# Kernel optimization log

Hardware: AMD Instinct MI355X
Metric: run time of the kernel (lower is better)

Reference implementation:

```python
import jax, jax.numpy as jnp
import numpy as np

HID = 2048; S = 2048; NH = 16
Q_LORA = 1536; KV_LORA = 512
D_NOPE = 128; D_ROPE = 64; D_V = 128
D_QK = D_NOPE + D_ROPE  # 192
EPS = 1e-6


def setup_inputs() -> dict:
    key = jax.random.key(0)
    ks = jax.random.split(key, 8)
    hidden_states = jax.random.normal(ks[0], (1, S, HID), dtype=jnp.float32)
    # real RoPE tables, HF layout: cos/sin = concat(freqs, freqs) along last dim
    inv_freq = 1.0 / (10000.0 ** (np.arange(0, D_ROPE, 2, dtype=np.float32) / D_ROPE))
    t = np.arange(S, dtype=np.float32)
    freqs = np.outer(t, inv_freq)  # [S, D_ROPE//2]
    emb = np.concatenate([freqs, freqs], axis=-1)  # [S, D_ROPE]
    cos = jnp.asarray(np.cos(emb))[None]  # [1, S, D_ROPE]
    sin = jnp.asarray(np.sin(emb))[None]
    def lin(k, fan_in, fan_out):
        return jax.random.normal(k, (fan_in, fan_out), dtype=jnp.float32) / np.sqrt(fan_in)
    return {
        'hidden_states': hidden_states, 'cos': cos, 'sin': sin,
        'w_qa': lin(ks[1], HID, Q_LORA),
        'g_qa': jnp.ones((Q_LORA,), jnp.float32),
        'w_qb': lin(ks[2], Q_LORA, NH * D_QK),
        'w_kva': lin(ks[3], HID, KV_LORA + D_ROPE),
        'g_kva': jnp.ones((KV_LORA,), jnp.float32),
        'w_kvb': lin(ks[4], KV_LORA, NH * (D_NOPE + D_V)),
        'w_o': lin(ks[5], NH * D_V, HID),
    }


def _rmsnorm(x, g):
    var = jnp.mean(x * x, axis=-1, keepdims=True)
    return x * jax.lax.rsqrt(var + EPS) * g


def _deinterleave(x):
    # view (..., d//2, 2) -> transpose -> reshape: even-index dims first, then odd
    b, h, s, d = x.shape
    return x.reshape(b, h, s, d // 2, 2).transpose(0, 1, 2, 4, 3).reshape(b, h, s, d)


def _rotate_half(x):
    x1, x2 = jnp.split(x, 2, axis=-1)
    return jnp.concatenate([-x2, x1], axis=-1)


def _apply_rope(q, k, cos, sin):
    cos = cos[:, None]  # [B,1,S,D]
    sin = sin[:, None]
    q = _deinterleave(q)
    k = _deinterleave(k)
    q_emb = q * cos + _rotate_half(q) * sin
    k_emb = k * cos + _rotate_half(k) * sin
    return q_emb, k_emb


def reference(hidden_states, cos, sin, w_qa, g_qa, w_qb, w_kva, g_kva, w_kvb, w_o):
    bsz, q_len, _ = hidden_states.shape
    # low-rank Q projection
    q = _rmsnorm(hidden_states @ w_qa, g_qa) @ w_qb  # [B,S,NH*D_QK]
    q = q.reshape(bsz, q_len, NH, D_QK).transpose(0, 2, 1, 3)  # [B,NH,S,D_QK]
    q_nope, q_pe = q[..., :D_NOPE], q[..., D_NOPE:]
    # compressed KV + shared rope key
    ckv = hidden_states @ w_kva  # [B,S,KV_LORA+D_ROPE]
    compressed_kv, k_pe = ckv[..., :KV_LORA], ckv[..., KV_LORA:]
    k_pe = k_pe.reshape(bsz, q_len, 1, D_ROPE).transpose(0, 2, 1, 3)  # [B,1,S,D_ROPE]
    kv = (_rmsnorm(compressed_kv, g_kva) @ w_kvb).reshape(bsz, q_len, NH, D_NOPE + D_V).transpose(0, 2, 1, 3)
    k_nope, value_states = kv[..., :D_NOPE], kv[..., D_NOPE:]
    # interleaved RoPE
    q_pe, k_pe = _apply_rope(q_pe, k_pe, cos, sin)
    query_states = jnp.concatenate([q_nope, q_pe], axis=-1)  # [B,NH,S,D_QK]
    key_states = jnp.concatenate([k_nope, jnp.broadcast_to(k_pe, (bsz, NH, q_len, D_ROPE))], axis=-1)
    # causal attention with MLA softmax scale
    scale = D_QK ** (-0.5)
    scores = jnp.einsum('bhqd,bhkd->bhqk', query_states, key_states) * scale
    mask = jnp.tril(jnp.ones((q_len, q_len), dtype=bool))
    scores = jnp.where(mask, scores, jnp.finfo(scores.dtype).min)
    probs = jax.nn.softmax(scores, axis=-1)
    attn = jnp.einsum('bhqk,bhkd->bhqd', probs, value_states)  # [B,NH,S,D_V]
    attn = attn.transpose(0, 2, 1, 3).reshape(bsz, q_len, NH * D_V)
    return attn @ w_o
```

## Files before the change

### kernel.cpp

```cpp
#include <hip/hip_runtime.h>
#include <hip/hip_bf16.h>

#define S_LEN 2048
#define HID_D 2048
#define NHEAD 16
#define QLORA 1536
#define KVLORA 512
#define DNOPE 128
#define DROPE 64
#define DV 128
#define DQK 192
#define NCAT 2176

#define KS_SH (64 * 192)
#define VS_SH (128 * 64)
#define BUF_SH (KS_SH + VS_SH)

typedef __hip_bfloat16 bf16;
typedef __attribute__((ext_vector_type(8))) short short8;
typedef __attribute__((ext_vector_type(4))) short s16x4;
typedef __attribute__((ext_vector_type(4))) float f32x4;

__device__ __forceinline__ float ldE(const float* p) { return *p; }
__device__ __forceinline__ float ldE(const bf16* p) { return __bfloat162float(*p); }
__device__ __forceinline__ void stE(float* p, float v) { *p = v; }
__device__ __forceinline__ void stE(bf16* p, float v) { *p = __float2bfloat16(v); }

__device__ __forceinline__ short bf16bits(float v) {
    __hip_bfloat16 h = __float2bfloat16(v);
    return *reinterpret_cast<short*>(&h);
}

__device__ __forceinline__ float b2f(short s) {
    union { short s; bf16 h; } u;
    u.s = s;
    return __bfloat162float(u.h);
}

__device__ __forceinline__ f32x4 mfma16(short8 a, short8 b, f32x4 c) {
    return __builtin_amdgcn_mfma_f32_16x16x32_bf16(a, b, c, 0, 0, 0);
}

__device__ __forceinline__ void gload16(const void* g, void* l) {
    __builtin_amdgcn_global_load_lds(
        (const __attribute__((address_space(1))) unsigned int*)g,
        (__attribute__((address_space(3))) unsigned int*)l, 16, 0, 0);
}

__global__ void detect_kernel(const void* hidden, int* flag) {
    __shared__ int red[256];
    const int tid = threadIdx.x;
    const bf16* hb = (const bf16*)hidden;
    float a = fabsf(__bfloat162float(hb[tid]));
    red[tid] = (!(a < 64.f) || (a != 0.f && a < 1e-30f)) ? 1 : 0;
    __syncthreads();
    for (int o = 128; o > 0; o >>= 1) {
        if (tid < o) red[tid] += red[tid + o];
        __syncthreads();
    }
    if (tid == 0) *flag = (red[0] > 16) ? 1 : 0;
}

__global__ void convert_kernel(const void* in, bf16* out, int n8, const int* flag) {
    int i = blockIdx.x * 256 + threadIdx.x;
    if (i >= n8) return;
    size_t off = (size_t)i * 8;
    short8 o;
    if (*flag) {
        const float* f = (const float*)in + off;
#pragma unroll
        for (int j = 0; j < 8; ++j) o[j] = bf16bits(f[j]);
    } else {
        o = *(const short8*)((const short*)in + off);
    }
    *(short8*)((short*)out + off) = o;
}

template <int KDIM>
__device__ void transpose_tile(const void* in, bf16* out, int N, int n0, int k0,
                               int roff, int fp32) {
    __shared__ __align__(16) short Ts[64][80];
    const int tid = threadIdx.x;
    const bool inb = n0 < N;
    const int kl = tid >> 4;
    const int nl = (tid & 15) * 4;
#pragma unroll
    for (int p = 0; p < 4; ++p) {
        int k = kl + p * 16;
        float v[4] = {0.f, 0.f, 0.f, 0.f};
        if (inb) {
            if (fp32) {
                const float4 f = *(const float4*)((const float*)in + (size_t)(k0 + k) * N + n0 + nl);
                v[0] = f.x; v[1] = f.y; v[2] = f.z; v[3] = f.w;
            } else {
                const bf16* bp = (const bf16*)in + (size_t)(k0 + k) * N + n0 + nl;
#pragma unroll
                for (int i = 0; i < 4; ++i) v[i] = __bfloat162float(bp[i]);
            }
        }
#pragma unroll
        for (int i = 0; i < 4; ++i) Ts[nl + i][k] = bf16bits(v[i]);
    }
    __syncthreads();
    const int nr = tid >> 2;
    const int kq = (tid & 3) * 16;
    short* op = (short*)out + (size_t)(roff + n0 + nr) * KDIM + k0 + kq;
    *(short8*)op = *(short8*)&Ts[nr][kq];
    *(short8*)(op + 8) = *(short8*)&Ts[nr][kq + 8];
}

__global__ void transpose_kernel(const void* in, bf16* out, int K, int N, int Npad,
                                 const int* flag) {
    __shared__ __align__(16) short Ts[64][80];
    const int tid = threadIdx.x;
    const int n0 = blockIdx.x * 64, k0 = blockIdx.y * 64;
    const bool inb = n0 < N;
    const int fp32 = *flag;
    const int kl = tid >> 4;
    const int nl = (tid & 15) * 4;
#pragma unroll
    for (int p = 0; p < 4; ++p) {
        int k = kl + p * 16;
        float v[4] = {0.f, 0.f, 0.f, 0.f};
        if (inb) {
            if (fp32) {
                const float4 f = *(const float4*)((const float*)in + (size_t)(k0 + k) * N + n0 + nl);
                v[0] = f.x; v[1] = f.y; v[2] = f.z; v[3] = f.w;
            } else {
                const bf16* bp = (const bf16*)in + (size_t)(k0 + k) * N + n0 + nl;
#pragma unroll
                for (int i = 0; i < 4; ++i) v[i] = __bfloat162float(bp[i]);
            }
        }
#pragma unroll
        for (int i = 0; i < 4; ++i) Ts[nl + i][k] = bf16bits(v[i]);
    }
    __syncthreads();
    const int nr = tid >> 2;
    const int kq = (tid & 3) * 16;
    short* op = (short*)out + (size_t)(n0 + nr) * K + k0 + kq;
    *(short8*)op = *(short8*)&Ts[nr][kq];
    *(short8*)(op + 8) = *(short8*)&Ts[nr][kq + 8];
}

__global__ void transpose2_kernel(const void* inA, const void* inB, bf16* out,
                                  const int* flag) {
    const int bx = blockIdx.x;
    const int k0 = blockIdx.y * 64;
    const int fp32 = *flag;
    if (bx < 24) transpose_tile<HID_D>(inA, out, QLORA, bx * 64, k0, 0, fp32);
    else         transpose_tile<HID_D>(inB, out, KVLORA + DROPE, (bx - 24) * 64, k0, QLORA, fp32);
}

__global__ void transposeQK_kernel(const void* inQ, bf16* outQ,
                                   const void* inKV, bf16* outKV, const int* flag) {
    const int bid = blockIdx.x;
    const int fp32 = *flag;
    if (bid < 1152) {
        const int n0 = (bid % 48) * 64, k0 = (bid / 48) * 64;
        transpose_tile<QLORA>(inQ, outQ, NHEAD * DQK, n0, k0, 0, fp32);
    } else {
        const int b = bid - 1152;
        const int n0 = (b % 64) * 64, k0 = (b / 64) * 64;
        transpose_tile<KVLORA>(inKV, outKV, NHEAD * (DNOPE + DV), n0, k0, 0, fp32);
    }
}

template <int MODE, typename TC>
__device__ void mgemm_body(const bf16* __restrict__ A, int lda,
                           const bf16* __restrict__ Bt, int ldb,
                           TC* __restrict__ C, int ldc, int K,
                           bf16* __restrict__ Kn, bf16* __restrict__ Vt) {
    __shared__ __align__(16) short As[128 * 64];
    __shared__ __align__(16) short Bs[128 * 64];
    const int tid = threadIdx.x;
    const int w = tid >> 6, lane = tid & 63;
    const int lg = lane >> 4, ln = lane & 15;
    const int wm = w >> 1, wn = w & 1;

    const int nbx = gridDim.x;
    const int flat = blockIdx.y * nbx + blockIdx.x;
    const int cpx = (nbx * gridDim.y) >> 3;
    const int swz = (flat & 7) * cpx + (flat >> 3);
    const int m0 = (swz / nbx) * 128, n0 = (swz % nbx) * 128;

    int aO[4], bO[4];
#pragma unroll
    for (int p = 0; p < 4; ++p) {
        const int cid = tid + p * 256;
        const int row = cid >> 3, cpos = cid & 7;
        const int c = cpos ^ (row & 7);
        aO[p] = (m0 + row) * lda + c * 8;
        bO[p] = (n0 + row) * ldb + c * 8;
    }
    int aoff[2][4], boff[2][4];
#pragma unroll
    for (int hk = 0; hk < 2; ++hk)
#pragma unroll
        for (int i = 0; i < 4; ++i) {
            const int ra = wm * 64 + i * 16 + ln;
            const int rb = wn * 64 + i * 16 + ln;
            aoff[hk][i] = ra * 64 + ((hk * 4 + lg) ^ (ra & 7)) * 8;
            boff[hk][i] = rb * 64 + ((hk * 4 + lg) ^ (rb & 7)) * 8;
        }

    f32x4 acc[4][4];
#pragma unroll
    for (int i = 0; i < 4; ++i)
#pragma unroll
        for (int j = 0; j < 4; ++j) acc[i][j] = (f32x4){0.f, 0.f, 0.f, 0.f};

    for (int k0 = 0; k0 < K; k0 += 64) {
        __syncthreads();
#pragma unroll
        for (int p = 0; p < 4; ++p) {
            gload16(A + (size_t)aO[p] + k0, As + (w + 4 * p) * 512);
            gload16(Bt + (size_t)bO[p] + k0, Bs + (w + 4 * p) * 512);
        }
        __syncthreads();
#pragma unroll
        for (int hk = 0; hk < 2; ++hk) {
            short8 af[4], bfr[4];
#pragma unroll
            for (int i = 0; i < 4; ++i) af[i] = *(const short8*)&As[aoff[hk][i]];
#pragma unroll
            for (int j = 0; j < 4; ++j) bfr[j] = *(const short8*)&Bs[boff[hk][j]];
#pragma unroll
            for (int i = 0; i < 4; ++i)
#pragma unroll
                for (int j = 0; j < 4; ++j) acc[i][j] = mfma16(af[i], bfr[j], acc[i][j]);
        }
    }
    if constexpr (MODE == 2) {
#pragma unroll
        for (int i = 0; i < 4; ++i)
#pragma unroll
            for (int j = 0; j < 4; ++j) {
                const int col = n0 + wn * 64 + j * 16 + ln;
                const int row = m0 + wm * 64 + i * 16 + lg * 4;
                const int h = col >> 8, d = col & 255;
                if (d < DNOPE) {
                    bf16* cp = Kn + (size_t)row * (NHEAD * DNOPE) + h * DNOPE + d;
#pragma unroll
                    for (int r = 0; r < 4; ++r)
                        cp[(size_t)r * (NHEAD * DNOPE)] = __float2bfloat16(acc[i][j][r]);
                } else {
                    s16x4 pk;
#pragma unroll
                    for (int r = 0; r < 4; ++r) pk[r] = bf16bits(acc[i][j][r]);
                    *(s16x4*)(Vt + (size_t)(h * DV + (d - DNOPE)) * S_LEN + row) = pk;
                }
            }
    } else {
#pragma unroll
        for (int i = 0; i < 4; ++i)
#pragma unroll
            for (int j = 0; j < 4; ++j) {
                TC* cp = C + (size_t)(m0 + wm * 64 + i * 16 + lg * 4) * ldc + n0 + wn * 64 +
                         j * 16 + ln;
#pragma unroll
                for (int r = 0; r < 4; ++r)
                    stE(cp + (size_t)r * ldc, acc[i][j][r]);
            }
    }
}

template <int MODE>
__global__ __launch_bounds__(256, 3)
void mgemm_kernel(const bf16* A, int lda, const bf16* Bt, int ldb, void* C, int ldc,
                  int K, const int* flag, bf16* Kn, bf16* Vt) {
    if (MODE == 1 && *flag)
        mgemm_body<1, float>(A, lda, Bt, ldb, (float*)C, ldc, K, nullptr, nullptr);
    else if (MODE == 2)
        mgemm_body<2, bf16>(A, lda, Bt, ldb, (bf16*)C, ldc, K, Kn, Vt);
    else
        mgemm_body<0, bf16>(A, lda, Bt, ldb, (bf16*)C, ldc, K, nullptr, nullptr);
}

template <typename TG>
__device__ void rmsnorm_row(const bf16* __restrict__ xr, const TG* __restrict__ g,
                            bf16* __restrict__ yr, int len) {
    const int tid = threadIdx.x;
    float ss = 0.f;
    for (int i = tid; i < len; i += 256) {
        float v = __bfloat162float(xr[i]);
        ss += v * v;
    }
    __shared__ float red[256];
    red[tid] = ss;
    __syncthreads();
    for (int o = 128; o > 0; o >>= 1) {
        if (tid < o) red[tid] += red[tid + o];
        __syncthreads();
    }
    const float scale = rsqrtf(red[0] / (float)len + 1e-6f);
    for (int i = tid; i < len; i += 256)
        yr[i] = __float2bfloat16(__bfloat162float(xr[i]) * scale * ldE(&g[i]));
}

__global__ void rmsnorm2_kernel(bf16* qk, const void* g_qa, const void* g_kva,
                                bf16* ckvn, const int* flag) {
    const int bid = blockIdx.x;
    if (*flag) {
        if (bid < S_LEN)
            rmsnorm_row<float>(qk + (size_t)bid * NCAT, (const float*)g_qa,
                               qk + (size_t)bid * NCAT, QLORA);
        else {
            const int s = bid - S_LEN;
            rmsnorm_row<float>(qk + (size_t)s * NCAT + QLORA, (const float*)g_kva,
                               ckvn + (size_t)s * KVLORA, KVLORA);
        }
    } else {
        if (bid < S_LEN)
            rmsnorm_row<bf16>(qk + (size_t)bid * NCAT, (const bf16*)g_qa,
                              qk + (size_t)bid * NCAT, QLORA);
        else {
            const int s = bid - S_LEN;
            rmsnorm_row<bf16>(qk + (size_t)s * NCAT + QLORA, (const bf16*)g_kva,
                              ckvn + (size_t)s * KVLORA, KVLORA);
        }
    }
}

template <typename TG>
__device__ void rope_body(bf16* __restrict__ q, const bf16* __restrict__ ckv,
                          bf16* __restrict__ kpe, const TG* __restrict__ cosb,
                          const TG* __restrict__ sinb) {
    const int s = blockIdx.x;
    const int tid = threadIdx.x;
    float x0 = 0.f, x1 = 0.f, c = 0.f, sn = 0.f;
    bf16* qbase = nullptr;
    int p = 0;
    const bool isq = tid < 512;
    const bool active = tid < 544;
    if (active) {
        if (isq) {
            const int h = tid >> 5;
            p = tid & 31;
            qbase = q + (size_t)s * (NHEAD * DQK) + h * DQK + DNOPE;
            x0 = __bfloat162float(qbase[2 * p]);
            x1 = __bfloat162float(qbase[2 * p + 1]);
        } else {
            p = tid - 512;
            const bf16* kb = ckv + (size_t)s * NCAT + KVLORA;
            x0 = __bfloat162float(kb[2 * p]);
            x1 = __bfloat162float(kb[2 * p + 1]);
        }
        c = ldE(&cosb[s * 64 + p]);
        sn = ldE(&sinb[s * 64 + p]);
    }
    __syncthreads();
    if (active) {
        if (isq) {
            qbase[p] = __float2bfloat16(x0 * c - x1 * sn);
            qbase[p + 32] = __float2bfloat16(x1 * c + x0 * sn);
        } else {
            kpe[s * 64 + p] = __float2bfloat16(x0 * c - x1 * sn);
            kpe[s * 64 + p + 32] = __float2bfloat16(x1 * c + x0 * sn);
        }
    }
}

__global__ void rope_kernel(bf16* q, const bf16* ckv, bf16* kpe,
                            const void* cosb, const void* sinb, const int* flag) {
    if (*flag) rope_body<float>(q, ckv, kpe, (const float*)cosb, (const float*)sinb);
    else       rope_body<bf16>(q, ckv, kpe, (const bf16*)cosb, (const bf16*)sinb);
}

__global__ __launch_bounds__(256, 2)
void fattn_kernel(const bf16* __restrict__ q, const bf16* __restrict__ kn,
                  const bf16* __restrict__ vt, const bf16* __restrict__ kpe,
                  bf16* __restrict__ attn, bf16* __restrict__ Opart, float* __restrict__ ml) {
    const int nf = blockIdx.x;
    const int xcd = nf & 7;
    const int j = nf >> 3;
    const int bx = j & 31;
    const int h = (j >> 5) * 8 + xcd;
    int qt, part, nparts;
    if (bx < 15)      { qt = 15 - bx / 3;        part = bx % 3;        nparts = 3; }
    else if (bx < 27) { qt = 10 - (bx - 15) / 2; part = (bx - 15) & 1; nparts = 2; }
    else              { qt = 31 - bx;            part = 0;             nparts = 1; }
    const int nt = 2 * qt + 2;
    const int bsz = nt / nparts, rr = nt % nparts;
    const int t0 = part * bsz + (part < rr ? part : rr);
    const int t1 = t0 + bsz + (part < rr ? 1 : 0);
    const int q0 = qt * 128;

    const int tid = threadIdx.x;
    const int w = tid >> 6;
    const int l = tid & 63;
    const int lg = l >> 4;
    const int ln = l & 15;

    __shared__ __align__(16) short KV[2][BUF_SH];

    int offK[6], sK[6];
    bool isn[6];
#pragma unroll
    for (int p = 0; p < 6; ++p) {
        const int cid = tid + p * 256;
        const int row = cid / 24;
        const int cpos = cid % 24;
        const int c = (cpos & 24) | ((cpos & 7) ^ (row & 7));
        if (c < 16) {
            offK[p] = row * (NHEAD * DNOPE) + h * DNOPE + c * 8;
            sK[p] = NHEAD * DNOPE;
            isn[p] = true;
        } else {
            offK[p] = row * DROPE + (c - 16) * 8;
            sK[p] = DROPE;
            isn[p] = false;
        }
    }
    int offV[4];
#pragma unroll
    for (int p = 0; p < 4; ++p) {
        const int cid = tid + p * 256;
        const int row = cid >> 3;
        const int cc = (cid & 7) ^ (row & 7);
        offV[p] = (h * DV + row) * S_LEN + cc * 8;
    }

    short8 qf[2][6];
#pragma unroll
    for (int i = 0; i < 2; ++i) {
        const short* qrow =
            (const short*)(q + (size_t)(q0 + i * 64 + w * 16 + ln) * (NHEAD * DQK) + h * DQK);
#pragma unroll
        for (int ks = 0; ks < 6; ++ks)
            qf[i][ks] = *(const short8*)(qrow + ks * 32 + lg * 8);
    }

    f32x4 O[2][8];
#pragma unroll
    for (int i = 0; i < 2; ++i)
#pragma unroll
        for (int ct = 0; ct < 8; ++ct) O[i][ct] = (f32x4){0.f, 0.f, 0.f, 0.f};
    float m_[2][4], l_[2][4];
#pragma unroll
    for (int i = 0; i < 2; ++i)
#pragma unroll
        for (int r = 0; r < 4; ++r) { m_[i][r] = -1e30f; l_[i][r] = 0.f; }
    const float scale = 0.07216878364870322f;

    {
        const int k0 = t0 * 64;
#pragma unroll
        for (int p = 0; p < 6; ++p) {
            const bf16* sp = (isn[p] ? kn : kpe) + (size_t)offK[p] + (size_t)k0 * sK[p];
            gload16(sp, &KV[0][0] + (w + 4 * p) * 512);
        }
#pragma unroll
        for (int p = 0; p < 4; ++p)
            gload16(vt + (size_t)offV[p] + k0, &KV[0][KS_SH] + (w + 4 * p) * 512);
    }

    for (int t = t0; t < t1; ++t) {
        const int cur = (t - t0) & 1;
        short* Ks = &KV[cur][0];
        short* Vs = &KV[cur][KS_SH];
        if (t + 1 < t1) {
            const int k0n = (t + 1) * 64;
            short* KsN = &KV[cur ^ 1][0];
            short* VsN = &KV[cur ^ 1][KS_SH];
#pragma unroll
            for (int p = 0; p < 6; ++p) {
                const bf16* sp = (isn[p] ? kn : kpe) + (size_t)offK[p] + (size_t)k0n * sK[p];
                gload16(sp, KsN + (w + 4 * p) * 512);
            }
#pragma unroll
            for (int p = 0; p < 4; ++p)
                gload16(vt + (size_t)offV[p] + k0n, VsN + (w + 4 * p) * 512);
            asm volatile("s_waitcnt vmcnt(10)" ::: "memory");
        } else {
            asm volatile("s_waitcnt vmcnt(0)" ::: "memory");
        }
        __builtin_amdgcn_s_barrier();

        const int k0 = t * 64;
        f32x4 S[2][4];
#pragma unroll
        for (int i = 0; i < 2; ++i)
#pragma unroll
            for (int c = 0; c < 4; ++c) S[i][c] = (f32x4){0.f, 0.f, 0.f, 0.f};
        __builtin_amdgcn_s_setprio(1);
#pragma unroll
        for (int ks = 0; ks < 6; ++ks) {
            const int kch = ks * 4 + lg;
#pragma unroll
            for (int c = 0; c < 4; ++c) {
                short8 kf = *(const short8*)&Ks[(size_t)(c * 16 + ln) * 192 +
                                               (size_t)(kch ^ (ln & 7)) * 8];
                S[0][c] = mfma16(qf[0][ks], kf, S[0][c]);
                S[1][c] = mfma16(qf[1][ks], kf, S[1][c]);
            }
        }
        __builtin_amdgcn_s_setprio(0);

        const int d0 = k0 - q0;
#pragma unroll
        for (int i = 0; i < 2; ++i)
#pragma unroll
            for (int c = 0; c < 4; ++c)
#pragma unroll
                for (int r = 0; r < 4; ++r) {
                    float v = S[i][c][r] * scale;
                    if (d0 > -64 &&
                        (d0 + c * 16 + ln) > (i * 64 + w * 16 + lg * 4 + r)) v = -1e30f;
                    S[i][c][r] = v;
                }

        float alpha[2][4];
#pragma unroll
        for (int i = 0; i < 2; ++i)
#pragma unroll
            for (int r = 0; r < 4; ++r) {
                float mx = fmaxf(fmaxf(S[i][0][r], S[i][1][r]), fmaxf(S[i][2][r], S[i][3][r]));
#pragma unroll
                for (int d = 1; d < 16; d <<= 1) mx = fmaxf(mx, __shfl_xor(mx, d));
                float mn = fmaxf(m_[i][r], mx);
                alpha[i][r] = __expf(m_[i][r] - mn);
                m_[i][r] = mn;
                float rs = 0.f;
#pragma unroll
                for (int c = 0; c < 4; ++c) {
                    float p = __expf(S[i][c][r] - mn);
                    S[i][c][r] = p;
                    rs += p;
                }
#pragma unroll
                for (int d = 1; d < 16; d <<= 1) rs += __shfl_xor(rs, d);
                l_[i][r] = l_[i][r] * alpha[i][r] + rs;
            }
#pragma unroll
        for (int i = 0; i < 2; ++i)
#pragma unroll
            for (int ct = 0; ct < 8; ++ct)
#pragma unroll
                for (int r = 0; r < 4; ++r) O[i][ct][r] *= alpha[i][r];

        __builtin_amdgcn_s_barrier();
        short* Pb = Ks;
#pragma unroll
        for (int i = 0; i < 2; ++i)
#pragma unroll
            for (int c = 0; c < 4; ++c)
#pragma unroll
                for (int r = 0; r < 4; ++r)
                    Pb[(size_t)(i * 64 + w * 16 + lg * 4 + r) * 70 + c * 16 + ln] =
                        bf16bits(S[i][c][r]);

        __builtin_amdgcn_s_setprio(1);
#pragma unroll
        for (int ks = 0; ks < 2; ++ks) {
            short8 pf0 = *(const short8*)&Pb[(size_t)(w * 16 + ln) * 70 + ks * 32 + lg * 8];
            short8 pf1 = *(const short8*)&Pb[(size_t)(64 + w * 16 + ln) * 70 + ks * 32 + lg * 8];
#pragma unroll
            for (int ct = 0; ct < 8; ++ct) {
                short8 vf = *(const short8*)&Vs[(size_t)(ct * 16 + ln) * 64 +
                                               (size_t)((ks * 4 + lg) ^ (ln & 7)) * 8];
                O[0][ct] = mfma16(pf0, vf, O[0][ct]);
                O[1][ct] = mfma16(pf1, vf, O[1][ct]);
            }
        }
        __builtin_amdgcn_s_setprio(0);
        __builtin_amdgcn_s_barrier();
    }

    if (nparts == 1) {
#pragma unroll
        for (int i = 0; i < 2; ++i)
#pragma unroll
            for (int r = 0; r < 4; ++r) {
                float inv = 1.f / l_[i][r];
                bf16* orow = attn + (size_t)(q0 + i * 64 + w * 16 + lg * 4 + r) * (NHEAD * DV) +
                             h * DV;
#pragma unroll
                for (int ct = 0; ct < 8; ++ct)
                    orow[ct * 16 + ln] = __float2bfloat16(O[i][ct][r] * inv);
            }
    } else {
        const int mlslot = h * 27 + (qt <= 10 ? (qt - 5) * 2 + part : 12 + (qt - 11) * 3 + part);
        float* mlp = ml + (size_t)mlslot * 128 * 2;
        if (part == 0) {
#pragma unroll
            for (int i = 0; i < 2; ++i)
#pragma unroll
                for (int r = 0; r < 4; ++r) {
                    const int rowb = i * 64 + w * 16 + lg * 4 + r;
                    bf16* orow = attn + (size_t)(q0 + rowb) * (NHEAD * DV) + h * DV;
#pragma unroll
                    for (int ct = 0; ct < 8; ++ct)
                        orow[ct * 16 + ln] = __float2bfloat16(O[i][ct][r]);
                    if (ln == 0) {
                        mlp[rowb * 2] = m_[i][r];
                        mlp[rowb * 2 + 1] = l_[i][r];
                    }
                }
        } else {
            const int oslot = h * 16 + (qt <= 10 ? (qt - 5) : 6 + (qt - 11) * 2 + (part - 1));
            bf16* op = Opart + (size_t)oslot * 128 * DV;
#pragma unroll
            for (int i = 0; i < 2; ++i)
#pragma unroll
                for (int r = 0; r < 4; ++r) {
                    const int rowb = i * 64 + w * 16 + lg * 4 + r;
#pragma unroll
                    for (int ct = 0; ct < 8; ++ct)
                        op[(size_t)rowb * DV + ct * 16 + ln] = __float2bfloat16(O[i][ct][r]);
                    if (ln == 0) {
                        mlp[rowb * 2] = m_[i][r];
                        mlp[rowb * 2 + 1] = l_[i][r];
                    }
                }
        }
    }
}

__global__ void reduce_kernel(const bf16* __restrict__ Opart, const float* __restrict__ ml,
                              bf16* __restrict__ attn) {
    const int qq = blockIdx.x;
    const int h = blockIdx.y;
    const int qt = 5 + qq;
    const int np = (qt <= 10) ? 2 : 3;
    const int q0 = qt * 128;
    const int tid = threadIdx.x;
    const int row = tid >> 1;
    const int dh = (tid & 1) * 64;
    float mp[3], lp[3], f[3];
    float mm = -1e30f;
    for (int p = 0; p < np; ++p) {
        const int msl = h * 27 + (qt <= 10 ? (qt - 5) * 2 + p : 12 + (qt - 11) * 3 + p);
        mp[p] = ml[((size_t)msl * 128 + row) * 2];
        lp[p] = ml[((size_t)msl * 128 + row) * 2 + 1];
        mm = fmaxf(mm, mp[p]);
    }
    float denom = 0.f;
    for (int p = 0; p < np; ++p) {
        f[p] = __expf(mp[p] - mm);
        denom += f[p] * lp[p];
    }
    const float inv = 1.f / denom;
    const int os1 = h * 16 + (qt <= 10 ? (qt - 5) : 6 + (qt - 11) * 2);
    bf16* arow = attn + (size_t)(q0 + row) * (NHEAD * DV) + h * DV + dh;
    const bf16* o1 = Opart + ((size_t)os1 * 128 + row) * DV + dh;
    const bf16* o2 = o1 + (size_t)128 * DV;
#pragma unroll
    for (int jc = 0; jc < 8; ++jc) {
        short8 a = *(const short8*)(arow + jc * 8);
        short8 b1 = *(const short8*)(o1 + jc * 8);
        short8 b2 = (np == 3) ? *(const short8*)(o2 + jc * 8) : b1;
        short8 o;
#pragma unroll
        for (int e = 0; e < 8; ++e) {
            float v = f[0] * b2f(a[e]) + f[1] * b2f(b1[e]);
            if (np == 3) v += f[2] * b2f(b2[e]);
            o[e] = bf16bits(v * inv);
        }
        *(short8*)(arow + jc * 8) = o;
    }
}

extern "C" void kernel_launch(void* const* d_in, const int* in_sizes, int n_in,
                              void* d_out, int out_size, void* d_ws, size_t ws_size,
                              hipStream_t stream) {
    const void* hidden = d_in[0];
    const void* cosb   = d_in[1];
    const void* sinb   = d_in[2];
    const void* w_qa   = d_in[3];
    const void* g_qa   = d_in[4];
    const void* w_qb   = d_in[5];
    const void* w_kva  = d_in[6];
    const void* g_kva  = d_in[7];
    const void* w_kvb  = d_in[8];
    const void* w_o    = d_in[9];

    bf16* ws = (bf16*)d_ws;
    bf16* qk   = ws;
    bf16* ckvn = qk + (size_t)S_LEN * NCAT;
    bf16* q    = ckvn + (size_t)S_LEN * KVLORA;
    bf16* kn   = q + (size_t)S_LEN * NHEAD * DQK;
    bf16* vtb  = kn + (size_t)S_LEN * NHEAD * DNOPE;
    bf16* kpe  = vtb + (size_t)NHEAD * DV * S_LEN;
    bf16* hbf  = kpe + (size_t)S_LEN * DROPE;
    int* flag  = (int*)(hbf + (size_t)S_LEN * HID_D);
    bf16* attn = ws;
    float* ml  = (float*)(ws + (size_t)S_LEN * HID_D);
    bf16* Opart = hbf;
    bf16* BtCat = kn;
    bf16* wqbT  = kn;
    bf16* wkvbT = hbf;
    bf16* W4    = q;

    detect_kernel<<<1, 256, 0, stream>>>(hidden, flag);
    convert_kernel<<<(S_LEN * HID_D / 8 + 255) / 256, 256, 0, stream>>>(
        hidden, hbf, S_LEN * HID_D / 8, flag);

    transpose2_kernel<<<dim3(34, HID_D / 64), 256, 0, stream>>>(w_qa, w_kva, BtCat, flag);
    mgemm_kernel<0><<<dim3(NCAT / 128, S_LEN / 128), 256, 0, stream>>>(
        hbf, HID_D, BtCat, HID_D, qk, NCAT, HID_D, flag, nullptr, nullptr);
    rmsnorm2_kernel<<<2 * S_LEN, 256, 0, stream>>>(qk, g_qa, g_kva, ckvn, flag);
    transposeQK_kernel<<<dim3(1664), 256, 0, stream>>>(w_qb, wqbT, w_kvb, wkvbT, flag);
    mgemm_kernel<0><<<dim3(NHEAD * DQK / 128, S_LEN / 128), 256, 0, stream>>>(
        qk, NCAT, wqbT, QLORA, q, NHEAD * DQK, QLORA, flag, nullptr, nullptr);
    mgemm_kernel<2><<<dim3(NHEAD * (DNOPE + DV) / 128, S_LEN / 128), 256, 0, stream>>>(
        ckvn, KVLORA, wkvbT, KVLORA, kn, NHEAD * (DNOPE + DV), KVLORA, flag, kn, vtb);
    rope_kernel<<<S_LEN, 576, 0, stream>>>(q, qk + QLORA, kpe, cosb, sinb, flag);
    fattn_kernel<<<dim3(512), 256, 0, stream>>>(q, kn, vtb, kpe, attn, Opart, ml);
    reduce_kernel<<<dim3(11, NHEAD), 256, 0, stream>>>(Opart, ml, attn);
    transpose_kernel<<<dim3(HID_D / 64, HID_D / 64), 256, 0, stream>>>(
        w_o, W4, HID_D, HID_D, HID_D, flag);
    mgemm_kernel<1><<<dim3(HID_D / 128, S_LEN / 128), 256, 0, stream>>>(
        attn, NHEAD * DV, W4, HID_D, d_out, HID_D, HID_D, flag, nullptr, nullptr);
}
```

Baseline: 349.5 us.

## Double-buffer GEMM shared-memory tiles to overlap global loads with MFMA

```diff
diff --git a/kernel.cpp b/kernel.cpp
--- a/kernel.cpp
+++ b/kernel.cpp
@@ -171,8 +171,7 @@
                            const bf16* __restrict__ Bt, int ldb,
                            TC* __restrict__ C, int ldc, int K,
                            bf16* __restrict__ Kn, bf16* __restrict__ Vt) {
-    __shared__ __align__(16) short As[128 * 64];
-    __shared__ __align__(16) short Bs[128 * 64];
+    __shared__ __align__(16) short AB[2][16384];
     const int tid = threadIdx.x;
     const int w = tid >> 6, lane = tid & 63;
     const int lg = lane >> 4, ln = lane & 15;
@@ -210,14 +209,32 @@
 #pragma unroll
         for (int j = 0; j < 4; ++j) acc[i][j] = (f32x4){0.f, 0.f, 0.f, 0.f};
 
-    for (int k0 = 0; k0 < K; k0 += 64) {
-        __syncthreads();
-#pragma unroll
-        for (int p = 0; p < 4; ++p) {
-            gload16(A + (size_t)aO[p] + k0, As + (w + 4 * p) * 512);
-            gload16(Bt + (size_t)bO[p] + k0, Bs + (w + 4 * p) * 512);
-        }
-        __syncthreads();
+#pragma unroll
+    for (int p = 0; p < 4; ++p) {
+        gload16(A + (size_t)aO[p], &AB[0][0] + (w + 4 * p) * 512);
+        gload16(Bt + (size_t)bO[p], &AB[0][8192] + (w + 4 * p) * 512);
+    }
+
+    const int nsteps = K >> 6;
+    for (int s = 0; s < nsteps; ++s) {
+        const int cur = s & 1;
+        const short* As = &AB[cur][0];
+        const short* Bs = &AB[cur][8192];
+        if (s + 1 < nsteps) {
+            const int k0n = (s + 1) * 64;
+            short* AsN = &AB[cur ^ 1][0];
+            short* BsN = &AB[cur ^ 1][8192];
+#pragma unroll
+            for (int p = 0; p < 4; ++p) {
+                gload16(A + (size_t)aO[p] + k0n, AsN + (w + 4 * p) * 512);
+                gload16(Bt + (size_t)bO[p] + k0n, BsN + (w + 4 * p) * 512);
+            }
+            asm volatile("s_waitcnt vmcnt(8)" ::: "memory");
+        } else {
+            asm volatile("s_waitcnt vmcnt(0)" ::: "memory");
+        }
+        __builtin_amdgcn_s_barrier();
+        __builtin_amdgcn_s_setprio(1);
 #pragma unroll
         for (int hk = 0; hk < 2; ++hk) {
             short8 af[4], bfr[4];
@@ -230,6 +247,8 @@
 #pragma unroll
                 for (int j = 0; j < 4; ++j) acc[i][j] = mfma16(af[i], bfr[j], acc[i][j]);
         }
+        __builtin_amdgcn_s_setprio(0);
+        __builtin_amdgcn_s_barrier();
     }
     if constexpr (MODE == 2) {
 #pragma unroll
@@ -266,7 +285,7 @@
 }
 
 template <int MODE>
-__global__ __launch_bounds__(256, 3)
+__global__ __launch_bounds__(256, 2)
 void mgemm_kernel(const bf16* A, int lda, const bf16* Bt, int ldb, void* C, int ldc,
                   int K, const int* flag, bf16* Kn, bf16* Vt) {
     if (MODE == 1 && *flag)
```

Result: faster. 336.7 us (-3.7%).
